# Kernel optimization log

Hardware: AMD Instinct MI355X
Metric: run time of the kernel (lower is better)

## Reference

```python
import jax, jax.numpy as jnp
import numpy as np

N, E, IN, OUT, H = 100000, 1600000, 128, 128, 4
C = OUT // H
NEG_SLOPE = 0.2  # PyG GATConv default LeakyReLU slope
BN_EPS = 1e-5


def setup_inputs() -> dict:
    key = jax.random.key(0)
    k = jax.random.split(key, 6)
    x = jax.random.normal(k[0], (N, IN), dtype=jnp.float32)
    edge_index = jax.random.randint(k[1], (2, E), 0, N, dtype=jnp.int64)
    W = jax.random.normal(k[2], (IN, H * C), dtype=jnp.float32) / np.sqrt(IN)
    att_src = jax.random.normal(k[3], (H, C), dtype=jnp.float32) * 0.1
    att_dst = jax.random.normal(k[4], (H, C), dtype=jnp.float32) * 0.1
    gat_bias = jnp.zeros((H * C,), dtype=jnp.float32)
    bn_gamma = jnp.ones((OUT,), dtype=jnp.float32)
    bn_beta = jnp.zeros((OUT,), dtype=jnp.float32)
    return {"x": x, "edge_index": edge_index, "W": W, "att_src": att_src,
            "att_dst": att_dst, "gat_bias": gat_bias, "bn_gamma": bn_gamma,
            "bn_beta": bn_beta}


def reference(x, edge_index, W, att_src, att_dst, gat_bias, bn_gamma, bn_beta):
    n = x.shape[0]
    # GATConv: linear transform, per-head view [N,H,C]
    h = (x @ W).reshape(n, H, C)
    # add self loops (PyG default add_self_loops=True)
    loop = jnp.arange(n, dtype=edge_index.dtype)
    src = jnp.concatenate([edge_index[0], loop])  # message source j
    dst = jnp.concatenate([edge_index[1], loop])  # message target i
    # per-node attention logits [N,H]
    a_src = jnp.einsum('nhc,hc->nh', h, att_src)
    a_dst = jnp.einsum('nhc,hc->nh', h, att_dst)
    # per-edge logits [Etot,H], LeakyReLU, segment softmax over dst
    e = jax.nn.leaky_relu(a_src[src] + a_dst[dst], NEG_SLOPE)
    m = jax.ops.segment_max(e, dst, num_segments=n)
    e = jnp.exp(e - m[dst])
    s = jax.ops.segment_sum(e, dst, num_segments=n)
    alpha = e / (s[dst] + 1e-16)  # dropout(p=0.3) is identity at eval
    # weighted scatter-add aggregation
    msg = h[src] * alpha[:, :, None]  # [Etot,H,C]
    out = jax.ops.segment_sum(msg, dst, num_segments=n).reshape(n, H * C)
    out = out + gat_bias
    # BatchNorm1d (batch statistics, biased var)
    mean = jnp.mean(out, axis=0)
    var = jnp.var(out, axis=0)
    out = bn_gamma * (out - mean) * jax.lax.rsqrt(var + BN_EPS) + bn_beta
    # residual (proj is Identity since in_ch == out_ch) + ReLU
    return jax.nn.relu(out + x)
```

## Files before the change

### kernel.cpp

```cpp
#include <hip/hip_runtime.h>

#define NEG 0.2f
#define EPB 8192
#define NB64MAX 1568
#define CAPB_MAX 1536

typedef short short8 __attribute__((ext_vector_type(8)));
typedef float floatx4 __attribute__((ext_vector_type(4)));

__device__ __forceinline__ float bf_lo(unsigned int u) { return __uint_as_float(u << 16); }
__device__ __forceinline__ float bf_hi(unsigned int u) { return __uint_as_float(u & 0xffff0000u); }
__device__ __forceinline__ unsigned short f2bf(float f) {
    unsigned int u = __float_as_uint(f);
    return (unsigned short)((u + 0x7fff + ((u >> 16) & 1)) >> 16);
}

__global__ __launch_bounds__(256) void k_wconv(const float* __restrict__ W,
                                               unsigned short* __restrict__ Wtb) {
    int i = blockIdx.x * 256 + threadIdx.x;
    int n = i >> 7, k = i & 127;
    Wtb[n * 128 + k] = f2bf(W[k * 128 + n]);
}

__global__ __launch_bounds__(256) void k_gemm(const float* __restrict__ x,
                                              const unsigned short* __restrict__ Wtb,
                                              const float* __restrict__ att_src,
                                              const float* __restrict__ att_dst,
                                              unsigned short* __restrict__ hb,
                                              unsigned int* __restrict__ asd, int N) {
    __shared__ unsigned short As[64 * 128];
    __shared__ unsigned short Bs[128 * 128];
    int t = threadIdx.x;
    int r0 = blockIdx.x * 64;
#pragma unroll
    for (int p = 0; p < 8; p++) {
        int idx = t + 256 * p;
        int row = idx >> 5, c4 = idx & 31;
        float4 v = make_float4(0.f, 0.f, 0.f, 0.f);
        if (r0 + row < N) v = *(const float4*)&x[(size_t)(r0 + row) * 128 + c4 * 4];
        int kb = c4 >> 1;
        unsigned short* d = &As[row * 128 + ((kb ^ (row & 7)) << 3) + (c4 & 1) * 4];
        d[0] = f2bf(v.x); d[1] = f2bf(v.y); d[2] = f2bf(v.z); d[3] = f2bf(v.w);
    }
#pragma unroll
    for (int p = 0; p < 8; p++) {
        int idx = t + 256 * p;
        int n = idx >> 4, k8 = idx & 15;
        *(short8*)&Bs[n * 128 + ((k8 ^ (n & 7)) << 3)] = *(const short8*)&Wtb[n * 128 + k8 * 8];
    }
    __syncthreads();
    int lane = t & 63, wv = t >> 6;
    int m16 = lane & 15, quad = lane >> 4;
    int rowbase = wv * 16;
    floatx4 acc[8];
#pragma unroll
    for (int c = 0; c < 8; c++) acc[c] = (floatx4){0.f, 0.f, 0.f, 0.f};
#pragma unroll
    for (int ks = 0; ks < 4; ks++) {
        int arow = rowbase + m16;
        short8 a = *(const short8*)&As[arow * 128 + (((ks * 4 + quad) ^ (arow & 7)) << 3)];
#pragma unroll
        for (int c = 0; c < 8; c++) {
            int brow = c * 16 + m16;
            short8 b = *(const short8*)&Bs[brow * 128 + (((ks * 4 + quad) ^ (brow & 7)) << 3)];
            acc[c] = __builtin_amdgcn_mfma_f32_16x16x32_bf16(a, b, acc[c], 0, 0, 0);
        }
    }
    float ps[4][4], pd[4][4];
#pragma unroll
    for (int hd = 0; hd < 4; hd++)
#pragma unroll
        for (int r = 0; r < 4; r++) { ps[hd][r] = 0.f; pd[hd][r] = 0.f; }
#pragma unroll
    for (int c = 0; c < 8; c++) {
        int col = c * 16 + m16;
        float as_ = att_src[col], ad_ = att_dst[col];
        int hd = c >> 1;
#pragma unroll
        for (int r = 0; r < 4; r++) {
            float v = acc[c][r];
            int row = r0 + rowbase + quad * 4 + r;
            if (row < N) hb[(size_t)row * 128 + col] = f2bf(v);
            ps[hd][r] = fmaf(v, as_, ps[hd][r]);
            pd[hd][r] = fmaf(v, ad_, pd[hd][r]);
        }
    }
#pragma unroll
    for (int off = 1; off < 16; off <<= 1) {
#pragma unroll
        for (int hd = 0; hd < 4; hd++)
#pragma unroll
            for (int r = 0; r < 4; r++) {
                ps[hd][r] += __shfl_xor(ps[hd][r], off, 16);
                pd[hd][r] += __shfl_xor(pd[hd][r], off, 16);
            }
    }
    if (m16 == 0) {
#pragma unroll
        for (int r = 0; r < 4; r++) {
            int row = r0 + rowbase + quad * 4 + r;
            if (row < N)
#pragma unroll
                for (int hd = 0; hd < 4; hd++)
                    asd[row * 4 + hd] = ((unsigned int)f2bf(pd[hd][r]) << 16) | f2bf(ps[hd][r]);
        }
    }
}

__global__ __launch_bounds__(512) void k_bin3(const int* __restrict__ ei,
                                              int* __restrict__ gcur,
                                              unsigned int* __restrict__ pairs,
                                              int E, int NB, int CAPB) {
    __shared__ int cnt[NB64MAX];
    __shared__ int lbase[NB64MAX];
    int t = threadIdx.x;
    for (int i = t; i < NB; i += 512) cnt[i] = 0;
    __syncthreads();
    int base = blockIdx.x * EPB, end = min(base + EPB, E);
    for (int i = base + t; i < end; i += 512) atomicAdd(&cnt[ei[E + i] >> 6], 1);
    __syncthreads();
    for (int i = t; i < NB; i += 512) {
        int c = cnt[i];
        if (c) {
            int s = atomicAdd(&gcur[i], c);
            lbase[i] = (s + c <= CAPB) ? s : -1;
        }
    }
    __syncthreads();
    for (int i = base + t; i < end; i += 512) {
        int d = ei[E + i];
        int b = d >> 6;
        int lb = lbase[b];
        if (lb >= 0) {
            int slot = atomicSub(&cnt[b], 1) - 1;
            pairs[(size_t)b * CAPB + lb + slot] =
                (unsigned int)ei[i] | ((unsigned int)(d & 63) << 20);
        }
    }
}

__global__ __launch_bounds__(256) void k_agg2(const unsigned int* __restrict__ hb,
                                              const unsigned int* __restrict__ asd,
                                              const int* __restrict__ gcur,
                                              const unsigned int* __restrict__ pairs,
                                              unsigned int* __restrict__ yb,
                                              int N, int CAPB) {
    __shared__ unsigned int ent[CAPB_MAX];
    __shared__ int cnt64[64], off64[64], cur64[64], stmp[64];
    int b = blockIdx.x, t = threadIdx.x;
    size_t base = (size_t)b * CAPB;
    int cnt = min(gcur[b], CAPB);
    if (t < 64) cnt64[t] = 0;
    __syncthreads();
    for (int i = t; i < cnt; i += 256) atomicAdd(&cnt64[(pairs[base + i] >> 20) & 63], 1);
    __syncthreads();
    if (t < 64) stmp[t] = cnt64[t];
    __syncthreads();
    for (int d = 1; d < 64; d <<= 1) {
        int add = (t < 64 && t >= d) ? stmp[t - d] : 0;
        __syncthreads();
        if (t < 64) stmp[t] += add;
        __syncthreads();
    }
    if (t < 64) { int ex = stmp[t] - cnt64[t]; off64[t] = ex; cur64[t] = ex; }
    __syncthreads();
    for (int i = t; i < cnt; i += 256) {
        unsigned int e = pairs[base + i];
        int slot = atomicAdd(&cur64[(e >> 20) & 63], 1);
        ent[slot] = e & 0xFFFFFu;
    }
    __syncthreads();
    int lane = t & 63, wv = t >> 6;
    int head = lane >> 4, sub = lane & 15, wsel = lane & 48;
    for (int k = 0; k < 16; k++) {
        int ln = wv * 16 + k;
        int n = b * 64 + ln;
        if (n >= N) break;
        unsigned int au = asd[n * 4 + head];
        float adst = bf_hi(au);
        float e0 = bf_lo(au) + adst;
        e0 = e0 > 0.f ? e0 : NEG * e0;
        float w0 = __expf(e0);
        unsigned int hu = hb[(size_t)n * 64 + lane];
        float acc0 = w0 * bf_lo(hu), acc1 = w0 * bf_hi(hu), sw = w0;
        int st = off64[ln], c = cnt64[ln];
        int sjn = n;
        float evn = 0.f;
        if (sub < c) {
            sjn = (int)ent[st + sub];
            evn = bf_lo(asd[sjn * 4 + head]);
        }
        for (int eb = 0; eb < c; eb += 16) {
            int sj_l = sjn;
            float ev = evn + adst;
            ev = ev > 0.f ? ev : NEG * ev;
            float wl = (eb + sub < c) ? __expf(ev) : 0.f;
            if (eb + 16 + sub < c) {
                sjn = (int)ent[st + eb + 16 + sub];
                evn = bf_lo(asd[sjn * 4 + head]);
            } else sjn = n;
#pragma unroll
            for (int j = 0; j < 16; j++) {
                int sj = __shfl(sj_l, j, 64);
                float wj = __shfl(wl, wsel | j, 64);
                unsigned int hj = hb[(size_t)sj * 64 + lane];
                acc0 = fmaf(wj, bf_lo(hj), acc0);
                acc1 = fmaf(wj, bf_hi(hj), acc1);
                sw += wj;
            }
        }
        float inv = 1.0f / (sw + 1e-16f);
        yb[(size_t)n * 64 + lane] = ((unsigned int)f2bf(acc1 * inv) << 16) | f2bf(acc0 * inv);
    }
}

__global__ __launch_bounds__(256) void k_bnstats(const unsigned int* __restrict__ yb,
                                                 float* __restrict__ gsum,
                                                 float* __restrict__ gsumsq, int N) {
    __shared__ float s0[256], s1[256], s2[256], s3[256];
    int t = threadIdx.x;
    int cp = t & 63;
    int g = t >> 6;
    int r0 = blockIdx.x * 128 + g;
    float sl = 0.f, sh = 0.f, ql = 0.f, qh = 0.f;
#pragma unroll 4
    for (int i = 0; i < 32; i++) {
        int r = r0 + i * 4;
        if (r < N) {
            unsigned int u = yb[(size_t)r * 64 + cp];
            float lo = bf_lo(u), hi = bf_hi(u);
            sl += lo; sh += hi;
            ql = fmaf(lo, lo, ql);
            qh = fmaf(hi, hi, qh);
        }
    }
    s0[t] = sl; s1[t] = sh; s2[t] = ql; s3[t] = qh;
    __syncthreads();
    if (t < 64) {
        float a = s0[t] + s0[t + 64] + s0[t + 128] + s0[t + 192];
        float bb = s1[t] + s1[t + 64] + s1[t + 128] + s1[t + 192];
        float c = s2[t] + s2[t + 64] + s2[t + 128] + s2[t + 192];
        float d = s3[t] + s3[t + 64] + s3[t + 128] + s3[t + 192];
        atomicAdd(&gsum[2 * t], a);
        atomicAdd(&gsum[2 * t + 1], bb);
        atomicAdd(&gsumsq[2 * t], c);
        atomicAdd(&gsumsq[2 * t + 1], d);
    }
}

__global__ __launch_bounds__(128) void k_bnfinal(const float* __restrict__ gsum,
                                                 const float* __restrict__ gsumsq,
                                                 const float* __restrict__ gamma,
                                                 const float* __restrict__ beta,
                                                 float* __restrict__ scale,
                                                 float* __restrict__ shift, int N) {
    int c = threadIdx.x;
    if (c < 128) {
        float invN = 1.0f / (float)N;
        float mean = gsum[c] * invN;
        float var = gsumsq[c] * invN - mean * mean;
        float sc = gamma[c] * rsqrtf(var + 1e-5f);
        scale[c] = sc;
        shift[c] = beta[c] - mean * sc;
    }
}

__global__ __launch_bounds__(256) void k_final(const unsigned int* __restrict__ yb,
                                               const float* __restrict__ x,
                                               const float* __restrict__ scale,
                                               const float* __restrict__ shift,
                                               float* __restrict__ out, int total4) {
    int i = blockIdx.x * 256 + threadIdx.x;
    if (i >= total4) return;
    int c4 = i & 31;
    uint2 u = ((const uint2*)yb)[i];
    float4 xv = ((const float4*)x)[i];
    float4 sc = ((const float4*)scale)[c4];
    float4 sh = ((const float4*)shift)[c4];
    float4 r;
    r.x = fmaxf(fmaf(bf_lo(u.x), sc.x, sh.x) + xv.x, 0.f);
    r.y = fmaxf(fmaf(bf_hi(u.x), sc.y, sh.y) + xv.y, 0.f);
    r.z = fmaxf(fmaf(bf_lo(u.y), sc.z, sh.z) + xv.z, 0.f);
    r.w = fmaxf(fmaf(bf_hi(u.y), sc.w, sh.w) + xv.w, 0.f);
    ((float4*)out)[i] = r;
}

extern "C" void kernel_launch(void* const* d_in, const int* in_sizes, int n_in,
                              void* d_out, int out_size, void* d_ws, size_t ws_size,
                              hipStream_t stream) {
    const float* x       = (const float*)d_in[0];
    const int*   ei      = (const int*)d_in[1];
    const float* W       = (const float*)d_in[2];
    const float* att_src = (const float*)d_in[3];
    const float* att_dst = (const float*)d_in[4];
    const float* gamma   = (const float*)d_in[6];
    const float* beta    = (const float*)d_in[7];
    int N = in_sizes[0] / 128;
    int E = in_sizes[1] / 2;
    int NB = (N + 63) / 64;

    char* base = (char*)d_ws;
    size_t off = 0;
    auto alloc = [&](size_t b) -> char* {
        char* p = base + off;
        off = (off + b + 255) & ~(size_t)255;
        return p;
    };
    unsigned short* hb  = (unsigned short*)alloc((size_t)N * 128 * 2);
    unsigned int*   yb  = (unsigned int*)alloc((size_t)N * 64 * 4);
    unsigned int*   asd = (unsigned int*)alloc((size_t)N * 4 * 4);
    unsigned short* Wtb = (unsigned short*)alloc(128 * 128 * 2);
    int*   gcur   = (int*)alloc((size_t)NB * 4);
    float* gsum   = (float*)alloc(512);
    float* gsumsq = (float*)alloc(512);
    float* scale  = (float*)alloc(512);
    float* shift  = (float*)alloc(512);
    size_t rem = (ws_size > off) ? (ws_size - off) : 0;
    int CAPB = (int)((rem / ((size_t)NB * 4)) & ~(size_t)15);
    if (CAPB > CAPB_MAX) CAPB = CAPB_MAX;
    unsigned int* pairs = (unsigned int*)alloc((size_t)NB * CAPB * 4);
    float* outp = (float*)d_out;

    hipMemsetAsync(gcur, 0, (size_t)NB * 4, stream);
    hipMemsetAsync(gsum, 0, 512, stream);
    hipMemsetAsync(gsumsq, 0, 512, stream);

    int chunks = (E + EPB - 1) / EPB;
    k_wconv<<<64, 256, 0, stream>>>(W, Wtb);
    k_gemm<<<(N + 63) / 64, 256, 0, stream>>>(x, Wtb, att_src, att_dst, hb, asd, N);
    k_bin3<<<chunks, 512, 0, stream>>>(ei, gcur, pairs, E, NB, CAPB);
    k_agg2<<<NB, 256, 0, stream>>>((const unsigned int*)hb, asd, gcur, pairs, yb, N, CAPB);
    k_bnstats<<<(N + 127) / 128, 256, 0, stream>>>(yb, gsum, gsumsq, N);
    k_bnfinal<<<1, 128, 0, stream>>>(gsum, gsumsq, gamma, beta, scale, shift, N);
    k_final<<<(N * 32 + 255) / 256, 256, 0, stream>>>(yb, x, scale, shift, outp, N * 32);
}
```

Before: 326.8 us.

## Fuse BN statistics into aggregation and precompute edge weights in shared memory

The aggregation kernel now computes all four per-head attention weights once per edge during binning, stores them as packed fp16 in shared memory, and pads each destination's edge list to a multiple of four. The inner loop then uses vectorized LDS reads and four independent gathers with two accumulator sets, replacing the per-edge shuffle and exp work. The BatchNorm sum and sum-of-squares reduction moves into the aggregation epilogue, which removes the separate stats kernel and its re-read of yb. In exchange the block uses more shared memory, which may lower occupancy, and the weights lose precision from fp16 storage. The fixed six-slot per-thread register buffer assumes at most 1536 edges per block.

Result: slower. 339.3 us (+3.8%).

```diff
diff --git a/kernel.cpp b/kernel.cpp
--- a/kernel.cpp
+++ b/kernel.cpp
@@ -1,9 +1,11 @@
 #include <hip/hip_runtime.h>
+#include <hip/hip_fp16.h>
 
 #define NEG 0.2f
 #define EPB 8192
 #define NB64MAX 1568
 #define CAPB_MAX 1536
+#define ENT_MAX 1728
 
 typedef short short8 __attribute__((ext_vector_type(8)));
 typedef float floatx4 __attribute__((ext_vector_type(4)));
@@ -13,6 +15,22 @@
 __device__ __forceinline__ unsigned short f2bf(float f) {
     unsigned int u = __float_as_uint(f);
     return (unsigned short)((u + 0x7fff + ((u >> 16) & 1)) >> 16);
+}
+__device__ __forceinline__ float lw(float e) {
+    e = e > 0.f ? e : NEG * e;
+    return __expf(e);
+}
+__device__ __forceinline__ unsigned int pkh2(float a, float b) {
+    __half2 h = __floats2half2_rn(a, b);
+    unsigned int u;
+    __builtin_memcpy(&u, &h, 4);
+    return u;
+}
+__device__ __forceinline__ float uph(unsigned int u, int shift) {
+    unsigned short s = (unsigned short)(u >> shift);
+    __half h;
+    __builtin_memcpy(&h, &s, 2);
+    return __half2float(h);
 }
 
 __global__ __launch_bounds__(256) void k_wconv(const float* __restrict__ W,
@@ -144,17 +162,41 @@
                                               const int* __restrict__ gcur,
                                               const unsigned int* __restrict__ pairs,
                                               unsigned int* __restrict__ yb,
+                                              float* __restrict__ gsum,
+                                              float* __restrict__ gsumsq,
                                               int N, int CAPB) {
-    __shared__ unsigned int ent[CAPB_MAX];
+    __shared__ __align__(16) unsigned int entS[ENT_MAX];
+    __shared__ __align__(16) unsigned int wpk[2][ENT_MAX];
     __shared__ int cnt64[64], off64[64], cur64[64], stmp[64];
+    __shared__ float adstS[64][4];
+    __shared__ float asrcS[64][4];
     int b = blockIdx.x, t = threadIdx.x;
     size_t base = (size_t)b * CAPB;
     int cnt = min(gcur[b], CAPB);
-    if (t < 64) cnt64[t] = 0;
-    __syncthreads();
-    for (int i = t; i < cnt; i += 256) atomicAdd(&cnt64[(pairs[base + i] >> 20) & 63], 1);
-    __syncthreads();
-    if (t < 64) stmp[t] = cnt64[t];
+    if (t < 64) {
+        cnt64[t] = 0;
+        int n = b * 64 + t;
+        uint4 au = make_uint4(0u, 0u, 0u, 0u);
+        if (n < N) au = *(const uint4*)&asd[n * 4];
+        adstS[t][0] = bf_hi(au.x); asrcS[t][0] = bf_lo(au.x);
+        adstS[t][1] = bf_hi(au.y); asrcS[t][1] = bf_lo(au.y);
+        adstS[t][2] = bf_hi(au.z); asrcS[t][2] = bf_lo(au.z);
+        adstS[t][3] = bf_hi(au.w); asrcS[t][3] = bf_lo(au.w);
+    }
+    __syncthreads();
+    unsigned int pe[6];
+#pragma unroll
+    for (int q = 0; q < 6; q++) {
+        int i = t + q * 256;
+        unsigned int e = 0xFFFFFFFFu;
+        if (i < cnt) {
+            e = pairs[base + i];
+            atomicAdd(&cnt64[(e >> 20) & 63], 1);
+        }
+        pe[q] = e;
+    }
+    __syncthreads();
+    if (t < 64) stmp[t] = (cnt64[t] + 3) & ~3;
     __syncthreads();
     for (int d = 1; d < 64; d <<= 1) {
         int add = (t < 64 && t >= d) ? stmp[t - d] : 0;
@@ -162,89 +204,94 @@
         if (t < 64) stmp[t] += add;
         __syncthreads();
     }
-    if (t < 64) { int ex = stmp[t] - cnt64[t]; off64[t] = ex; cur64[t] = ex; }
-    __syncthreads();
-    for (int i = t; i < cnt; i += 256) {
-        unsigned int e = pairs[base + i];
-        int slot = atomicAdd(&cur64[(e >> 20) & 63], 1);
-        ent[slot] = e & 0xFFFFFu;
+    if (t < 64) {
+        int ex = stmp[t] - ((cnt64[t] + 3) & ~3);
+        off64[t] = ex;
+        cur64[t] = ex;
+    }
+    __syncthreads();
+#pragma unroll
+    for (int q = 0; q < 6; q++) {
+        unsigned int e = pe[q];
+        if (e != 0xFFFFFFFFu) {
+            int ln = (e >> 20) & 63;
+            unsigned int sj = e & 0xFFFFFu;
+            int slot = atomicAdd(&cur64[ln], 1);
+            entS[slot] = sj;
+            uint4 au = *(const uint4*)&asd[sj * 4];
+            float w0 = lw(bf_lo(au.x) + adstS[ln][0]);
+            float w1 = lw(bf_lo(au.y) + adstS[ln][1]);
+            float w2 = lw(bf_lo(au.z) + adstS[ln][2]);
+            float w3 = lw(bf_lo(au.w) + adstS[ln][3]);
+            wpk[0][slot] = pkh2(w0, w1);
+            wpk[1][slot] = pkh2(w2, w3);
+        }
+    }
+    __syncthreads();
+    if (t < 64) {
+        int cn = cnt64[t], st = off64[t];
+        int padded = (cn + 3) & ~3;
+        for (int i = cn; i < padded; i++) {
+            entS[st + i] = 0u;
+            wpk[0][st + i] = 0u;
+            wpk[1][st + i] = 0u;
+        }
     }
     __syncthreads();
     int lane = t & 63, wv = t >> 6;
-    int head = lane >> 4, sub = lane & 15, wsel = lane & 48;
+    int head = lane >> 4;
+    int hpl = head >> 1;
+    int hsh = (head & 1) * 16;
+    const unsigned int* wplane = wpk[hpl];
+    float t_sl = 0.f, t_sh = 0.f, t_ql = 0.f, t_qh = 0.f;
+#pragma unroll 1
     for (int k = 0; k < 16; k++) {
         int ln = wv * 16 + k;
         int n = b * 64 + ln;
         if (n >= N) break;
-        unsigned int au = asd[n * 4 + head];
-        float adst = bf_hi(au);
-        float e0 = bf_lo(au) + adst;
+        float e0 = asrcS[ln][head] + adstS[ln][head];
         e0 = e0 > 0.f ? e0 : NEG * e0;
         float w0 = __expf(e0);
-        unsigned int hu = hb[(size_t)n * 64 + lane];
-        float acc0 = w0 * bf_lo(hu), acc1 = w0 * bf_hi(hu), sw = w0;
+        unsigned int hu = hb[(unsigned)(n * 64 + lane)];
+        float a0A = w0 * bf_lo(hu), a1A = w0 * bf_hi(hu), swA = w0;
+        float a0B = 0.f, a1B = 0.f, swB = 0.f;
         int st = off64[ln], c = cnt64[ln];
-        int sjn = n;
-        float evn = 0.f;
-        if (sub < c) {
-            sjn = (int)ent[st + sub];
-            evn = bf_lo(asd[sjn * 4 + head]);
-        }
-        for (int eb = 0; eb < c; eb += 16) {
-            int sj_l = sjn;
-            float ev = evn + adst;
-            ev = ev > 0.f ? ev : NEG * ev;
-            float wl = (eb + sub < c) ? __expf(ev) : 0.f;
-            if (eb + 16 + sub < c) {
-                sjn = (int)ent[st + eb + 16 + sub];
-                evn = bf_lo(asd[sjn * 4 + head]);
-            } else sjn = n;
-#pragma unroll
-            for (int j = 0; j < 16; j++) {
-                int sj = __shfl(sj_l, j, 64);
-                float wj = __shfl(wl, wsel | j, 64);
-                unsigned int hj = hb[(size_t)sj * 64 + lane];
-                acc0 = fmaf(wj, bf_lo(hj), acc0);
-                acc1 = fmaf(wj, bf_hi(hj), acc1);
-                sw += wj;
-            }
-        }
-        float inv = 1.0f / (sw + 1e-16f);
-        yb[(size_t)n * 64 + lane] = ((unsigned int)f2bf(acc1 * inv) << 16) | f2bf(acc0 * inv);
-    }
-}
-
-__global__ __launch_bounds__(256) void k_bnstats(const unsigned int* __restrict__ yb,
-                                                 float* __restrict__ gsum,
-                                                 float* __restrict__ gsumsq, int N) {
-    __shared__ float s0[256], s1[256], s2[256], s3[256];
-    int t = threadIdx.x;
-    int cp = t & 63;
-    int g = t >> 6;
-    int r0 = blockIdx.x * 128 + g;
-    float sl = 0.f, sh = 0.f, ql = 0.f, qh = 0.f;
-#pragma unroll 4
-    for (int i = 0; i < 32; i++) {
-        int r = r0 + i * 4;
-        if (r < N) {
-            unsigned int u = yb[(size_t)r * 64 + cp];
-            float lo = bf_lo(u), hi = bf_hi(u);
-            sl += lo; sh += hi;
-            ql = fmaf(lo, lo, ql);
-            qh = fmaf(hi, hi, qh);
-        }
-    }
-    s0[t] = sl; s1[t] = sh; s2[t] = ql; s3[t] = qh;
+        const unsigned int* ep = &entS[st];
+        const unsigned int* wp = &wplane[st];
+        for (int e = 0; e < c; e += 4) {
+            uint4 s4 = *(const uint4*)&ep[e];
+            uint4 w4 = *(const uint4*)&wp[e];
+            unsigned int h0 = hb[(s4.x << 6) | (unsigned)lane];
+            unsigned int h1 = hb[(s4.y << 6) | (unsigned)lane];
+            unsigned int h2 = hb[(s4.z << 6) | (unsigned)lane];
+            unsigned int h3 = hb[(s4.w << 6) | (unsigned)lane];
+            float wj0 = uph(w4.x, hsh), wj1 = uph(w4.y, hsh);
+            float wj2 = uph(w4.z, hsh), wj3 = uph(w4.w, hsh);
+            a0A = fmaf(wj0, bf_lo(h0), a0A); a1A = fmaf(wj0, bf_hi(h0), a1A); swA += wj0;
+            a0B = fmaf(wj1, bf_lo(h1), a0B); a1B = fmaf(wj1, bf_hi(h1), a1B); swB += wj1;
+            a0A = fmaf(wj2, bf_lo(h2), a0A); a1A = fmaf(wj2, bf_hi(h2), a1A); swA += wj2;
+            a0B = fmaf(wj3, bf_lo(h3), a0B); a1B = fmaf(wj3, bf_hi(h3), a1B); swB += wj3;
+        }
+        float inv = 1.0f / (swA + swB + 1e-16f);
+        float ylo = (a0A + a0B) * inv, yhi = (a1A + a1B) * inv;
+        yb[(unsigned)(n * 64 + lane)] = ((unsigned int)f2bf(yhi) << 16) | f2bf(ylo);
+        t_sl += ylo; t_sh += yhi;
+        t_ql = fmaf(ylo, ylo, t_ql);
+        t_qh = fmaf(ylo * 0.f + yhi, yhi, t_qh);
+    }
+    __syncthreads();
+    float* red = (float*)wpk;
+    red[t] = t_sl; red[256 + t] = t_sh; red[512 + t] = t_ql; red[768 + t] = t_qh;
     __syncthreads();
     if (t < 64) {
-        float a = s0[t] + s0[t + 64] + s0[t + 128] + s0[t + 192];
-        float bb = s1[t] + s1[t + 64] + s1[t + 128] + s1[t + 192];
-        float c = s2[t] + s2[t + 64] + s2[t + 128] + s2[t + 192];
-        float d = s3[t] + s3[t + 64] + s3[t + 128] + s3[t + 192];
+        float a = red[t] + red[t + 64] + red[t + 128] + red[t + 192];
+        float bb = red[256 + t] + red[256 + t + 64] + red[256 + t + 128] + red[256 + t + 192];
+        float cc = red[512 + t] + red[512 + t + 64] + red[512 + t + 128] + red[512 + t + 192];
+        float dd = red[768 + t] + red[768 + t + 64] + red[768 + t + 128] + red[768 + t + 192];
         atomicAdd(&gsum[2 * t], a);
         atomicAdd(&gsum[2 * t + 1], bb);
-        atomicAdd(&gsumsq[2 * t], c);
-        atomicAdd(&gsumsq[2 * t + 1], d);
+        atomicAdd(&gsumsq[2 * t], cc);
+        atomicAdd(&gsumsq[2 * t + 1], dd);
     }
 }
 
@@ -329,8 +376,8 @@
     k_wconv<<<64, 256, 0, stream>>>(W, Wtb);
     k_gemm<<<(N + 63) / 64, 256, 0, stream>>>(x, Wtb, att_src, att_dst, hb, asd, N);
     k_bin3<<<chunks, 512, 0, stream>>>(ei, gcur, pairs, E, NB, CAPB);
-    k_agg2<<<NB, 256, 0, stream>>>((const unsigned int*)hb, asd, gcur, pairs, yb, N, CAPB);
-    k_bnstats<<<(N + 127) / 128, 256, 0, stream>>>(yb, gsum, gsumsq, N);
+    k_agg2<<<NB, 256, 0, stream>>>((const unsigned int*)hb, asd, gcur, pairs, yb,
+                                   gsum, gsumsq, N, CAPB);
     k_bnfinal<<<1, 128, 0, stream>>>(gsum, gsumsq, gamma, beta, scale, shift, N);
     k_final<<<(N * 32 + 255) / 256, 256, 0, stream>>>(yb, x, scale, shift, outp, N * 32);
 }
```

## Fuse BN stats into aggregation, fold BN finalize into output, halve node bins

Applied to the files above, without the earlier changes.

Batch-norm statistics are now accumulated inside the aggregation kernel from the values it just wrote, which removes the separate stats pass that re-read the aggregated features. The scale/shift computation moves into the shared-memory prologue of the final kernel, removing the single-block finalize launch. Destination bins shrink from 64 to 32 nodes, which doubles the aggregation grid and gives each bin a smaller per-block edge buffer; pair entries are held in registers rather than re-read from memory. Costs: about 3k blocks doing global float atomics for the stats, every final block recomputing the 128 BN coefficients, and a lower bin capacity that could drop edges if a bin exceeds 896 entries.

Result: slower. 388.1 us (+18.8%).

```diff
diff --git a/kernel.cpp b/kernel.cpp
--- a/kernel.cpp
+++ b/kernel.cpp
@@ -2,8 +2,8 @@
 
 #define NEG 0.2f
 #define EPB 8192
-#define NB64MAX 1568
-#define CAPB_MAX 1536
+#define NBMAX 3136
+#define CAPB_MAX 896
 
 typedef short short8 __attribute__((ext_vector_type(8)));
 typedef float floatx4 __attribute__((ext_vector_type(4)));
@@ -111,13 +111,13 @@
                                               int* __restrict__ gcur,
                                               unsigned int* __restrict__ pairs,
                                               int E, int NB, int CAPB) {
-    __shared__ int cnt[NB64MAX];
-    __shared__ int lbase[NB64MAX];
+    __shared__ int cnt[NBMAX];
+    __shared__ int lbase[NBMAX];
     int t = threadIdx.x;
     for (int i = t; i < NB; i += 512) cnt[i] = 0;
     __syncthreads();
     int base = blockIdx.x * EPB, end = min(base + EPB, E);
-    for (int i = base + t; i < end; i += 512) atomicAdd(&cnt[ei[E + i] >> 6], 1);
+    for (int i = base + t; i < end; i += 512) atomicAdd(&cnt[ei[E + i] >> 5], 1);
     __syncthreads();
     for (int i = t; i < NB; i += 512) {
         int c = cnt[i];
@@ -129,12 +129,12 @@
     __syncthreads();
     for (int i = base + t; i < end; i += 512) {
         int d = ei[E + i];
-        int b = d >> 6;
+        int b = d >> 5;
         int lb = lbase[b];
         if (lb >= 0) {
             int slot = atomicSub(&cnt[b], 1) - 1;
             pairs[(size_t)b * CAPB + lb + slot] =
-                (unsigned int)ei[i] | ((unsigned int)(d & 63) << 20);
+                (unsigned int)ei[i] | ((unsigned int)(d & 31) << 20);
         }
     }
 }
@@ -144,46 +144,63 @@
                                               const int* __restrict__ gcur,
                                               const unsigned int* __restrict__ pairs,
                                               unsigned int* __restrict__ yb,
+                                              float* __restrict__ gsum,
+                                              float* __restrict__ gsumsq,
                                               int N, int CAPB) {
     __shared__ unsigned int ent[CAPB_MAX];
-    __shared__ int cnt64[64], off64[64], cur64[64], stmp[64];
+    __shared__ float red[1024];
+    __shared__ int cnt32[32], off32[32], cur32[32], stmp[32];
     int b = blockIdx.x, t = threadIdx.x;
     size_t base = (size_t)b * CAPB;
     int cnt = min(gcur[b], CAPB);
-    if (t < 64) cnt64[t] = 0;
-    __syncthreads();
-    for (int i = t; i < cnt; i += 256) atomicAdd(&cnt64[(pairs[base + i] >> 20) & 63], 1);
-    __syncthreads();
-    if (t < 64) stmp[t] = cnt64[t];
-    __syncthreads();
-    for (int d = 1; d < 64; d <<= 1) {
-        int add = (t < 64 && t >= d) ? stmp[t - d] : 0;
+    if (t < 32) cnt32[t] = 0;
+    __syncthreads();
+    unsigned int pe[4];
+#pragma unroll
+    for (int q = 0; q < 4; q++) {
+        int i = t + q * 256;
+        unsigned int e = 0xFFFFFFFFu;
+        if (i < cnt) {
+            e = pairs[base + i];
+            atomicAdd(&cnt32[(e >> 20) & 31], 1);
+        }
+        pe[q] = e;
+    }
+    __syncthreads();
+    if (t < 32) stmp[t] = cnt32[t];
+    __syncthreads();
+    for (int d = 1; d < 32; d <<= 1) {
+        int add = (t < 32 && t >= d) ? stmp[t - d] : 0;
         __syncthreads();
-        if (t < 64) stmp[t] += add;
+        if (t < 32) stmp[t] += add;
         __syncthreads();
     }
-    if (t < 64) { int ex = stmp[t] - cnt64[t]; off64[t] = ex; cur64[t] = ex; }
-    __syncthreads();
-    for (int i = t; i < cnt; i += 256) {
-        unsigned int e = pairs[base + i];
-        int slot = atomicAdd(&cur64[(e >> 20) & 63], 1);
-        ent[slot] = e & 0xFFFFFu;
+    if (t < 32) { int ex = stmp[t] - cnt32[t]; off32[t] = ex; cur32[t] = ex; }
+    __syncthreads();
+#pragma unroll
+    for (int q = 0; q < 4; q++) {
+        unsigned int e = pe[q];
+        if (e != 0xFFFFFFFFu) {
+            int slot = atomicAdd(&cur32[(e >> 20) & 31], 1);
+            ent[slot] = e & 0xFFFFFu;
+        }
     }
     __syncthreads();
     int lane = t & 63, wv = t >> 6;
     int head = lane >> 4, sub = lane & 15, wsel = lane & 48;
-    for (int k = 0; k < 16; k++) {
-        int ln = wv * 16 + k;
-        int n = b * 64 + ln;
+    float t_sl = 0.f, t_sh = 0.f, t_ql = 0.f, t_qh = 0.f;
+    for (int k = 0; k < 8; k++) {
+        int ln = wv * 8 + k;
+        int n = b * 32 + ln;
         if (n >= N) break;
         unsigned int au = asd[n * 4 + head];
         float adst = bf_hi(au);
         float e0 = bf_lo(au) + adst;
         e0 = e0 > 0.f ? e0 : NEG * e0;
         float w0 = __expf(e0);
-        unsigned int hu = hb[(size_t)n * 64 + lane];
+        unsigned int hu = hb[(unsigned)(n * 64 + lane)];
         float acc0 = w0 * bf_lo(hu), acc1 = w0 * bf_hi(hu), sw = w0;
-        int st = off64[ln], c = cnt64[ln];
+        int st = off32[ln], c = cnt32[ln];
         int sjn = n;
         float evn = 0.f;
         if (sub < c) {
@@ -203,85 +220,62 @@
             for (int j = 0; j < 16; j++) {
                 int sj = __shfl(sj_l, j, 64);
                 float wj = __shfl(wl, wsel | j, 64);
-                unsigned int hj = hb[(size_t)sj * 64 + lane];
+                unsigned int hj = hb[(unsigned)(sj * 64 + lane)];
                 acc0 = fmaf(wj, bf_lo(hj), acc0);
                 acc1 = fmaf(wj, bf_hi(hj), acc1);
                 sw += wj;
             }
         }
         float inv = 1.0f / (sw + 1e-16f);
-        yb[(size_t)n * 64 + lane] = ((unsigned int)f2bf(acc1 * inv) << 16) | f2bf(acc0 * inv);
-    }
-}
-
-__global__ __launch_bounds__(256) void k_bnstats(const unsigned int* __restrict__ yb,
-                                                 float* __restrict__ gsum,
-                                                 float* __restrict__ gsumsq, int N) {
-    __shared__ float s0[256], s1[256], s2[256], s3[256];
-    int t = threadIdx.x;
-    int cp = t & 63;
-    int g = t >> 6;
-    int r0 = blockIdx.x * 128 + g;
-    float sl = 0.f, sh = 0.f, ql = 0.f, qh = 0.f;
-#pragma unroll 4
-    for (int i = 0; i < 32; i++) {
-        int r = r0 + i * 4;
-        if (r < N) {
-            unsigned int u = yb[(size_t)r * 64 + cp];
-            float lo = bf_lo(u), hi = bf_hi(u);
-            sl += lo; sh += hi;
-            ql = fmaf(lo, lo, ql);
-            qh = fmaf(hi, hi, qh);
-        }
-    }
-    s0[t] = sl; s1[t] = sh; s2[t] = ql; s3[t] = qh;
+        unsigned int yw = ((unsigned int)f2bf(acc1 * inv) << 16) | f2bf(acc0 * inv);
+        yb[(unsigned)(n * 64 + lane)] = yw;
+        float ylo = bf_lo(yw), yhi = bf_hi(yw);
+        t_sl += ylo; t_sh += yhi;
+        t_ql = fmaf(ylo, ylo, t_ql);
+        t_qh = fmaf(yhi, yhi, t_qh);
+    }
+    red[t] = t_sl; red[256 + t] = t_sh; red[512 + t] = t_ql; red[768 + t] = t_qh;
     __syncthreads();
     if (t < 64) {
-        float a = s0[t] + s0[t + 64] + s0[t + 128] + s0[t + 192];
-        float bb = s1[t] + s1[t + 64] + s1[t + 128] + s1[t + 192];
-        float c = s2[t] + s2[t + 64] + s2[t + 128] + s2[t + 192];
-        float d = s3[t] + s3[t + 64] + s3[t + 128] + s3[t + 192];
+        float a = red[t] + red[t + 64] + red[t + 128] + red[t + 192];
+        float bb = red[256 + t] + red[256 + t + 64] + red[256 + t + 128] + red[256 + t + 192];
+        float cc = red[512 + t] + red[512 + t + 64] + red[512 + t + 128] + red[512 + t + 192];
+        float dd = red[768 + t] + red[768 + t + 64] + red[768 + t + 128] + red[768 + t + 192];
         atomicAdd(&gsum[2 * t], a);
         atomicAdd(&gsum[2 * t + 1], bb);
-        atomicAdd(&gsumsq[2 * t], c);
-        atomicAdd(&gsumsq[2 * t + 1], d);
-    }
-}
-
-__global__ __launch_bounds__(128) void k_bnfinal(const float* __restrict__ gsum,
-                                                 const float* __restrict__ gsumsq,
-                                                 const float* __restrict__ gamma,
-                                                 const float* __restrict__ beta,
-                                                 float* __restrict__ scale,
-                                                 float* __restrict__ shift, int N) {
-    int c = threadIdx.x;
-    if (c < 128) {
-        float invN = 1.0f / (float)N;
-        float mean = gsum[c] * invN;
-        float var = gsumsq[c] * invN - mean * mean;
-        float sc = gamma[c] * rsqrtf(var + 1e-5f);
-        scale[c] = sc;
-        shift[c] = beta[c] - mean * sc;
+        atomicAdd(&gsumsq[2 * t], cc);
+        atomicAdd(&gsumsq[2 * t + 1], dd);
     }
 }
 
 __global__ __launch_bounds__(256) void k_final(const unsigned int* __restrict__ yb,
                                                const float* __restrict__ x,
-                                               const float* __restrict__ scale,
-                                               const float* __restrict__ shift,
-                                               float* __restrict__ out, int total4) {
-    int i = blockIdx.x * 256 + threadIdx.x;
+                                               const float* __restrict__ gsum,
+                                               const float* __restrict__ gsumsq,
+                                               const float* __restrict__ gamma,
+                                               const float* __restrict__ beta,
+                                               float* __restrict__ out, int N, int total4) {
+    __shared__ float scS[128], shS[128];
+    int t = threadIdx.x;
+    if (t < 128) {
+        float invN = 1.0f / (float)N;
+        float mean = gsum[t] * invN;
+        float var = gsumsq[t] * invN - mean * mean;
+        float sc = gamma[t] * rsqrtf(var + 1e-5f);
+        scS[t] = sc;
+        shS[t] = beta[t] - mean * sc;
+    }
+    __syncthreads();
+    int i = blockIdx.x * 256 + t;
     if (i >= total4) return;
     int c4 = i & 31;
     uint2 u = ((const uint2*)yb)[i];
     float4 xv = ((const float4*)x)[i];
-    float4 sc = ((const float4*)scale)[c4];
-    float4 sh = ((const float4*)shift)[c4];
     float4 r;
-    r.x = fmaxf(fmaf(bf_lo(u.x), sc.x, sh.x) + xv.x, 0.f);
-    r.y = fmaxf(fmaf(bf_hi(u.x), sc.y, sh.y) + xv.y, 0.f);
-    r.z = fmaxf(fmaf(bf_lo(u.y), sc.z, sh.z) + xv.z, 0.f);
-    r.w = fmaxf(fmaf(bf_hi(u.y), sc.w, sh.w) + xv.w, 0.f);
+    r.x = fmaxf(fmaf(bf_lo(u.x), scS[c4 * 4 + 0], shS[c4 * 4 + 0]) + xv.x, 0.f);
+    r.y = fmaxf(fmaf(bf_hi(u.x), scS[c4 * 4 + 1], shS[c4 * 4 + 1]) + xv.y, 0.f);
+    r.z = fmaxf(fmaf(bf_lo(u.y), scS[c4 * 4 + 2], shS[c4 * 4 + 2]) + xv.z, 0.f);
+    r.w = fmaxf(fmaf(bf_hi(u.y), scS[c4 * 4 + 3], shS[c4 * 4 + 3]) + xv.w, 0.f);
     ((float4*)out)[i] = r;
 }
 
@@ -297,7 +291,7 @@
     const float* beta    = (const float*)d_in[7];
     int N = in_sizes[0] / 128;
     int E = in_sizes[1] / 2;
-    int NB = (N + 63) / 64;
+    int NB = (N + 31) / 32;
 
     char* base = (char*)d_ws;
     size_t off = 0;
@@ -313,8 +307,6 @@
     int*   gcur   = (int*)alloc((size_t)NB * 4);
     float* gsum   = (float*)alloc(512);
     float* gsumsq = (float*)alloc(512);
-    float* scale  = (float*)alloc(512);
-    float* shift  = (float*)alloc(512);
     size_t rem = (ws_size > off) ? (ws_size - off) : 0;
     int CAPB = (int)((rem / ((size_t)NB * 4)) & ~(size_t)15);
     if (CAPB > CAPB_MAX) CAPB = CAPB_MAX;
@@ -329,8 +321,8 @@
     k_wconv<<<64, 256, 0, stream>>>(W, Wtb);
     k_gemm<<<(N + 63) / 64, 256, 0, stream>>>(x, Wtb, att_src, att_dst, hb, asd, N);
     k_bin3<<<chunks, 512, 0, stream>>>(ei, gcur, pairs, E, NB, CAPB);
-    k_agg2<<<NB, 256, 0, stream>>>((const unsigned int*)hb, asd, gcur, pairs, yb, N, CAPB);
-    k_bnstats<<<(N + 127) / 128, 256, 0, stream>>>(yb, gsum, gsumsq, N);
-    k_bnfinal<<<1, 128, 0, stream>>>(gsum, gsumsq, gamma, beta, scale, shift, N);
-    k_final<<<(N * 32 + 255) / 256, 256, 0, stream>>>(yb, x, scale, shift, outp, N * 32);
-}
+    k_agg2<<<NB, 256, 0, stream>>>((const unsigned int*)hb, asd, gcur, pairs, yb,
+                                   gsum, gsumsq, N, CAPB);
+    k_final<<<(N * 32 + 255) / 256, 256, 0, stream>>>(yb, x, gsum, gsumsq, gamma, beta,
+                                                      outp, N, N * 32);
+}
```
